# Kernel tuning notes

Measured on AMD Instinct MI355X. Metric: run time of the kernel, lower is better.

Reference implementation:

```python
import jax, jax.numpy as jnp
import numpy as np

N = 8192       # tokens = batch x seq
D = 2048       # d_model
H = 2048       # per-expert hidden size
E = 8          # num_experts
TOP_K = 2


def setup_inputs() -> dict:
    key = jax.random.key(0)
    ks = jax.random.split(key, 6)
    x = jax.random.normal(ks[0], (N, D), dtype=jnp.float32)
    expert_weights = jax.random.uniform(ks[1], (N, TOP_K), dtype=jnp.float32)
    expert_indices = jax.random.randint(ks[2], (N, TOP_K), 0, E, dtype=jnp.int32)
    batch_size_per_expert = jnp.bincount(expert_indices.reshape(-1), length=E).astype(jnp.int32)
    scale = 0.02
    w1 = jax.random.normal(ks[3], (E, D, H), dtype=jnp.float32) * scale
    w2 = jax.random.normal(ks[4], (E, H, D), dtype=jnp.float32) * scale
    w3 = jax.random.normal(ks[5], (E, D, H), dtype=jnp.float32) * scale
    return {"x": x, "expert_weights": expert_weights, "expert_indices": expert_indices,
            "batch_size_per_expert": batch_size_per_expert, "w1": w1, "w2": w2, "w3": w3}


def reference(x, expert_weights, expert_indices, batch_size_per_expert, w1, w2, w3):
    """Math-equivalent to ParallelMLP.forward_once (non-EP path):
    sort tokens by expert, run per-expert SwiGLU MLP, unpermute and combine
    with top-k routing weights. Output does not depend on the sort order,
    so we express it as: out[t] = sum_k w[t,k] * expert_{idx[t,k]}(x[t]).
    """
    n, d = x.shape
    e = w1.shape[0]
    # Dense combine weights (n, E): scatter top-k routing weights.
    cw = jnp.zeros((n, e), x.dtype).at[jnp.arange(n)[:, None], expert_indices].add(expert_weights)
    out = jnp.zeros_like(x)
    for i in range(e):  # small fixed expert count
        h = jax.nn.silu(x @ w1[i]) * (x @ w3[i])  # (n, H) SwiGLU
        out = out + cw[:, i:i + 1] * (h @ w2[i])
    return out
```

## Files before the change

kernel.cpp:

```cpp
#include <hip/hip_runtime.h>
#include <stdint.h>

typedef unsigned short u16;
typedef __attribute__((ext_vector_type(8))) short s16x8;
typedef __attribute__((ext_vector_type(8))) unsigned short u16x8;
typedef __attribute__((ext_vector_type(4))) float f32x4;

#define N_TOK 8192
#define DDIM 2048
#define HDIM 2048
#define NROWS 16384
#define PADROWS 16640
#define MAXTILES 72
#define KTILES 32

#define W1T_OFF    0ull
#define W3T_OFF    67108864ull
#define W2T_OFF    134217728ull
#define XBF_OFF    201326592ull
#define HS_OFF     234881024ull
#define ROWTOK_OFF 303038464ull
#define POS_OFF    303107072ull
#define META_OFF   303172608ull
#define RES_OFF    0ull
#define WS_NEED    303172736ull

__device__ __forceinline__ u16 f2bf(float f) {
  union { float f; unsigned u; } v; v.f = f;
  unsigned r = v.u + 0x7fffu + ((v.u >> 16) & 1u);
  return (u16)(r >> 16);
}
__device__ __forceinline__ float bf2f(u16 u) {
  union { unsigned u; float f; } v; v.u = ((unsigned)u) << 16; return v.f;
}
__device__ __forceinline__ void gload_lds16(const u16* g, u16* l) {
  __builtin_amdgcn_global_load_lds(
      (const __attribute__((address_space(1))) unsigned int*)g,
      (__attribute__((address_space(3))) unsigned int*)l, 16, 0, 0);
}

__global__ void r1_kernel(const int* __restrict__ bsz, int* __restrict__ meta,
                          int* __restrict__ rowtok) {
  if (threadIdx.x == 0) {
    int off = 0, tbv = 0;
    meta[8] = 0; meta[17] = 0;
    for (int e = 0; e < 8; ++e) {
      meta[e] = 0;
      int c = bsz[e];
      off += c;  meta[9 + e] = off;
      tbv += (c + 255) >> 8; meta[18 + e] = tbv;
    }
  }
  for (int p = NROWS + (int)threadIdx.x; p < PADROWS; p += 256) rowtok[p] = 0;
}

__global__ void r2_kernel(const int* __restrict__ eidx, int* __restrict__ meta,
                          int* __restrict__ rowtok, int* __restrict__ posOf) {
  int i = blockIdx.x * 256 + threadIdx.x;
  int e = eidx[i];
  int p = atomicAdd(&meta[e], 1);
  int row = meta[8 + e] + p;
  rowtok[row] = i >> 1;
  posOf[i] = row;
}

__global__ void convert_x_kernel(const float* __restrict__ x, u16* __restrict__ xbf) {
  long long c = blockIdx.x * 256 + threadIdx.x;
  const float4 v0 = *(const float4*)&x[c * 8];
  const float4 v1 = *(const float4*)&x[c * 8 + 4];
  u16x8 u;
  u[0] = f2bf(v0.x); u[1] = f2bf(v0.y); u[2] = f2bf(v0.z); u[3] = f2bf(v0.w);
  u[4] = f2bf(v1.x); u[5] = f2bf(v1.y); u[6] = f2bf(v1.z); u[7] = f2bf(v1.w);
  *(u16x8*)&xbf[c * 8] = u;
}

__global__ __launch_bounds__(256) void transpose_cvt_kernel(
    const float* __restrict__ w1, const float* __restrict__ w2, const float* __restrict__ w3,
    u16* __restrict__ w1T, u16* __restrict__ w2T, u16* __restrict__ w3T) {
  __shared__ float tile[64][65];
  int z = blockIdx.z;
  const float* src; u16* dst;
  if (z < 8)        { src = w1 + (size_t)z * 4194304;        dst = w1T + (size_t)z * 4194304; }
  else if (z < 16)  { src = w3 + (size_t)(z - 8) * 4194304;  dst = w3T + (size_t)(z - 8) * 4194304; }
  else              { src = w2 + (size_t)(z - 16) * 4194304; dst = w2T + (size_t)(z - 16) * 4194304; }
  int r0 = blockIdx.y * 64, c0 = blockIdx.x * 64;
  int tid = threadIdx.x;
  int lr = tid >> 4, lc4 = (tid & 15) * 4;
#pragma unroll
  for (int i = 0; i < 4; ++i) {
    const float4 v = *(const float4*)&src[(size_t)(r0 + lr + i * 16) * 2048 + c0 + lc4];
    tile[lr + i * 16][lc4 + 0] = v.x; tile[lr + i * 16][lc4 + 1] = v.y;
    tile[lr + i * 16][lc4 + 2] = v.z; tile[lr + i * 16][lc4 + 3] = v.w;
  }
  __syncthreads();
  int orb = tid >> 3, oc8 = (tid & 7) * 8;
#pragma unroll
  for (int i = 0; i < 2; ++i) {
    int orow = orb + i * 32;
    u16x8 u;
#pragma unroll
    for (int j = 0; j < 8; ++j) u[j] = f2bf(tile[oc8 + j][orow]);
    *(u16x8*)&dst[(size_t)(c0 + orow) * 2048 + r0 + oc8] = u;
  }
}

template<int EPI>
__global__ __launch_bounds__(512, 2) void gemm_moe_kernel(
    const u16* __restrict__ A, const u16* __restrict__ B1m, const u16* __restrict__ B3m,
    const int* __restrict__ gather, const int* __restrict__ meta, u16* __restrict__ out) {
  const int* offs = meta + 8;
  const int* tb = meta + 17;

  const int nwg = (int)(gridDim.x * gridDim.y);
  const int lin = (int)(blockIdx.y * gridDim.x + blockIdx.x);
  const int q8 = nwg >> 3, r8 = nwg & 7;
  const int xcd = lin & 7, idx = lin >> 3;
  const int nl = (xcd < r8 ? xcd * (q8 + 1) : r8 * (q8 + 1) + (xcd - r8) * q8) + idx;
  const int tileId = nl % MAXTILES;
  const int colb = nl / MAXTILES;

  if (tileId >= tb[8]) return;
  int e = 0;
#pragma unroll
  for (int qq = 1; qq < 8; ++qq) if (tileId >= tb[qq]) e = qq;
  const int row0 = offs[e] + (tileId - tb[e]) * 256;
  const int vr = offs[e + 1] - row0;

  const int bRowA = EPI ? colb * 128 : colb * 256;
  const int bRowB = EPI ? colb * 128 : colb * 256 + 128;

  __shared__ u16 lds[2][4][8192];

  const int tid = threadIdx.x;
  const int wid = tid >> 6, lane = tid & 63;
  const int lm = lane & 15, kg = lane >> 4;
  const int wr = wid >> 2, wc = wid & 3;

  const u16* pA0[2]; const u16* pA1[2]; const u16* pB1[2]; const u16* pB3[2];
#pragma unroll
  for (int l = 0; l < 2; ++l) {
    int S = (wid * 2 + l) * 64 + lane;
    int r = S >> 3;
    int c8 = ((S & 7) ^ (r & 7)) * 8;
    int ga0 = row0 + r, ga1 = row0 + 128 + r;
    int ta0 = gather ? gather[ga0] : ga0;
    int ta1 = gather ? gather[ga1] : ga1;
    pA0[l] = A + (size_t)ta0 * 2048 + c8;
    pA1[l] = A + (size_t)ta1 * 2048 + c8;
    pB1[l] = B1m + ((size_t)e * 2048 + bRowA + r) * 2048 + c8;
    pB3[l] = B3m + ((size_t)e * 2048 + bRowB + r) * 2048 + c8;
  }

  int fA[2];
  fA[0] = lm * 64 + ((kg) ^ (lm & 7)) * 8;
  fA[1] = lm * 64 + ((4 + kg) ^ (lm & 7)) * 8;

  f32x4 acc1[8][2], acc3[8][2];
  f32x4 z4 = {0.f, 0.f, 0.f, 0.f};
#pragma unroll
  for (int m = 0; m < 8; ++m)
#pragma unroll
    for (int n = 0; n < 2; ++n) { acc1[m][n] = z4; acc3[m][n] = z4; }

#define STG(b, u, P) do { \
    gload_lds16(P[0], &lds[b][u][(wid * 2 + 0) * 512]); \
    gload_lds16(P[1], &lds[b][u][(wid * 2 + 1) * 512]); } while (0)
#define ADV() do { pA0[0]+=64; pA0[1]+=64; pA1[0]+=64; pA1[1]+=64; \
    pB1[0]+=64; pB1[1]+=64; pB3[0]+=64; pB3[1]+=64; } while (0)

  STG(0, 0, pA0); STG(0, 1, pA1); STG(0, 2, pB1); STG(0, 3, pB3);
  ADV();
  asm volatile("s_waitcnt vmcnt(0)" ::: "memory");
  __builtin_amdgcn_s_barrier();

  s16x8 a[4][2], b[2][2];

  for (int t = 0; t < KTILES; ++t) {
    const int cur = t & 1;
    const bool more = (t + 1 < KTILES);

#pragma unroll
    for (int mi = 0; mi < 4; ++mi)
#pragma unroll
      for (int kk = 0; kk < 2; ++kk)
        a[mi][kk] = *(const s16x8*)&lds[cur][wr][mi * 1024 + fA[kk]];
#pragma unroll
    for (int n = 0; n < 2; ++n)
#pragma unroll
      for (int kk = 0; kk < 2; ++kk)
        b[n][kk] = *(const s16x8*)&lds[cur][2][wc * 2048 + n * 1024 + fA[kk]];
    if (more) { STG(cur ^ 1, 0, pA0); STG(cur ^ 1, 2, pB1); }
    __builtin_amdgcn_s_barrier();
    __builtin_amdgcn_s_setprio(1);
#pragma unroll
    for (int mi = 0; mi < 4; ++mi)
#pragma unroll
      for (int n = 0; n < 2; ++n) {
        acc1[mi][n] = __builtin_amdgcn_mfma_f32_16x16x32_bf16(a[mi][0], b[n][0], acc1[mi][n], 0, 0, 0);
        acc1[mi][n] = __builtin_amdgcn_mfma_f32_16x16x32_bf16(a[mi][1], b[n][1], acc1[mi][n], 0, 0, 0);
      }
    __builtin_amdgcn_s_setprio(0);
    __builtin_amdgcn_s_barrier();

#pragma unroll
    for (int n = 0; n < 2; ++n)
#pragma unroll
      for (int kk = 0; kk < 2; ++kk)
        b[n][kk] = *(const s16x8*)&lds[cur][3][wc * 2048 + n * 1024 + fA[kk]];
    if (more) { STG(cur ^ 1, 1, pA1); STG(cur ^ 1, 3, pB3); }
    __builtin_amdgcn_s_barrier();
    __builtin_amdgcn_s_setprio(1);
#pragma unroll
    for (int mi = 0; mi < 4; ++mi)
#pragma unroll
      for (int n = 0; n < 2; ++n) {
        acc3[mi][n] = __builtin_amdgcn_mfma_f32_16x16x32_bf16(a[mi][0], b[n][0], acc3[mi][n], 0, 0, 0);
        acc3[mi][n] = __builtin_amdgcn_mfma_f32_16x16x32_bf16(a[mi][1], b[n][1], acc3[mi][n], 0, 0, 0);
      }
    __builtin_amdgcn_s_setprio(0);
    __builtin_amdgcn_s_barrier();

#pragma unroll
    for (int mi = 0; mi < 4; ++mi)
#pragma unroll
      for (int kk = 0; kk < 2; ++kk)
        a[mi][kk] = *(const s16x8*)&lds[cur][wr][(4 + mi) * 1024 + fA[kk]];
#pragma unroll
    for (int n = 0; n < 2; ++n)
#pragma unroll
      for (int kk = 0; kk < 2; ++kk)
        b[n][kk] = *(const s16x8*)&lds[cur][2][wc * 2048 + n * 1024 + fA[kk]];
    __builtin_amdgcn_s_barrier();
    __builtin_amdgcn_s_setprio(1);
#pragma unroll
    for (int mi = 0; mi < 4; ++mi)
#pragma unroll
      for (int n = 0; n < 2; ++n) {
        acc1[4 + mi][n] = __builtin_amdgcn_mfma_f32_16x16x32_bf16(a[mi][0], b[n][0], acc1[4 + mi][n], 0, 0, 0);
        acc1[4 + mi][n] = __builtin_amdgcn_mfma_f32_16x16x32_bf16(a[mi][1], b[n][1], acc1[4 + mi][n], 0, 0, 0);
      }
    __builtin_amdgcn_s_setprio(0);
    __builtin_amdgcn_s_barrier();

#pragma unroll
    for (int n = 0; n < 2; ++n)
#pragma unroll
      for (int kk = 0; kk < 2; ++kk)
        b[n][kk] = *(const s16x8*)&lds[cur][3][wc * 2048 + n * 1024 + fA[kk]];
    asm volatile("s_waitcnt vmcnt(0)" ::: "memory");
    __builtin_amdgcn_s_barrier();
    __builtin_amdgcn_s_setprio(1);
#pragma unroll
    for (int mi = 0; mi < 4; ++mi)
#pragma unroll
      for (int n = 0; n < 2; ++n) {
        acc3[4 + mi][n] = __builtin_amdgcn_mfma_f32_16x16x32_bf16(a[mi][0], b[n][0], acc3[4 + mi][n], 0, 0, 0);
        acc3[4 + mi][n] = __builtin_amdgcn_mfma_f32_16x16x32_bf16(a[mi][1], b[n][1], acc3[4 + mi][n], 0, 0, 0);
      }
    __builtin_amdgcn_s_setprio(0);
    __builtin_amdgcn_s_barrier();

    if (more) ADV();
  }

#pragma unroll
  for (int m = 0; m < 8; ++m)
#pragma unroll
    for (int n = 0; n < 2; ++n) {
      const int rloc = wr * 128 + m * 16 + kg * 4;
      if (EPI == 1) {
        const int col = colb * 128 + wc * 32 + n * 16 + lm;
#pragma unroll
        for (int rr = 0; rr < 4; ++rr) {
          int rowl = rloc + rr;
          if (rowl < vr) {
            float z = acc1[m][n][rr];
            float h = z / (1.f + __expf(-z)) * acc3[m][n][rr];
            out[(size_t)(row0 + rowl) * 2048 + col] = f2bf(h);
          }
        }
      } else {
        const int col = colb * 256 + wc * 32 + n * 16 + lm;
#pragma unroll
        for (int rr = 0; rr < 4; ++rr) {
          int rowl = rloc + rr;
          if (rowl < vr) {
            out[(size_t)(row0 + rowl) * 2048 + col] = f2bf(acc1[m][n][rr]);
            out[(size_t)(row0 + rowl) * 2048 + col + 128] = f2bf(acc3[m][n][rr]);
          }
        }
      }
    }
#undef STG
#undef ADV
}

__global__ void combine_kernel(const u16* __restrict__ res, const int* __restrict__ posOf,
                               const float* __restrict__ ew, float* __restrict__ out) {
  int c = blockIdx.x * 256 + threadIdx.x;
  int t = c >> 8, dc = (c & 255) * 8;
  int p0 = posOf[2 * t], p1 = posOf[2 * t + 1];
  float wa = ew[2 * t], wb = ew[2 * t + 1];
  u16x8 u0 = *(const u16x8*)&res[(size_t)p0 * 2048 + dc];
  u16x8 u1 = *(const u16x8*)&res[(size_t)p1 * 2048 + dc];
  float4 o0, o1;
  o0.x = wa * bf2f(u0[0]) + wb * bf2f(u1[0]);
  o0.y = wa * bf2f(u0[1]) + wb * bf2f(u1[1]);
  o0.z = wa * bf2f(u0[2]) + wb * bf2f(u1[2]);
  o0.w = wa * bf2f(u0[3]) + wb * bf2f(u1[3]);
  o1.x = wa * bf2f(u0[4]) + wb * bf2f(u1[4]);
  o1.y = wa * bf2f(u0[5]) + wb * bf2f(u1[5]);
  o1.z = wa * bf2f(u0[6]) + wb * bf2f(u1[6]);
  o1.w = wa * bf2f(u0[7]) + wb * bf2f(u1[7]);
  *(float4*)&out[(size_t)t * 2048 + dc] = o0;
  *(float4*)&out[(size_t)t * 2048 + dc + 4] = o1;
}

extern "C" void kernel_launch(void* const* d_in, const int* in_sizes, int n_in,
                              void* d_out, int out_size, void* d_ws, size_t ws_size,
                              hipStream_t stream) {
  const float* x  = (const float*)d_in[0];
  const float* ew = (const float*)d_in[1];
  const int* eidx = (const int*)d_in[2];
  const int* bsz  = (const int*)d_in[3];
  const float* w1 = (const float*)d_in[4];
  const float* w2 = (const float*)d_in[5];
  const float* w3 = (const float*)d_in[6];
  float* out = (float*)d_out;
  char* ws = (char*)d_ws;

  if (ws_size < WS_NEED) {
    hipMemsetAsync(d_out, 0, (size_t)out_size * 4, stream);
    return;
  }

  u16* w1T = (u16*)(ws + W1T_OFF);
  u16* w3T = (u16*)(ws + W3T_OFF);
  u16* w2T = (u16*)(ws + W2T_OFF);
  u16* xbf = (u16*)(ws + XBF_OFF);
  u16* hs  = (u16*)(ws + HS_OFF);
  u16* res = (u16*)(ws + RES_OFF);
  int* rowtok = (int*)(ws + ROWTOK_OFF);
  int* posOf  = (int*)(ws + POS_OFF);
  int* meta   = (int*)(ws + META_OFF);

  r1_kernel<<<1, 256, 0, stream>>>(bsz, meta, rowtok);
  r2_kernel<<<64, 256, 0, stream>>>(eidx, meta, rowtok, posOf);
  convert_x_kernel<<<8192, 256, 0, stream>>>(x, xbf);
  transpose_cvt_kernel<<<dim3(32, 32, 24), 256, 0, stream>>>(w1, w2, w3, w1T, w2T, w3T);
  gemm_moe_kernel<1><<<dim3(MAXTILES, 16), 512, 0, stream>>>(xbf, w1T, w3T, rowtok, meta, hs);
  gemm_moe_kernel<0><<<dim3(MAXTILES, 8), 512, 0, stream>>>(hs, w2T, w2T, nullptr, meta, res);
  combine_kernel<<<8192, 256, 0, stream>>>(res, posOf, ew, out);
}
```

Baseline: 762.9 us.

## Prefetch full next K-tile up front and cut barriers in MoE GEMM loop

The GEMM main loop is restructured so all eight global-to-LDS loads for the next K-tile are issued at the start of each iteration. A partial `s_waitcnt vmcnt(8)` then waits only for the current tile, and the loop body drops from eight barriers to three. B1 and B3 fragments are read from LDS together so each A fragment feeds both accumulators in one MFMA burst, and the last iteration is peeled off. This aims to reduce barrier stalls and give loads more time to overlap compute. The cost is extra live B registers under the 512x2 launch bound, which could cause spills or lower occupancy.

```diff
diff --git a/kernel.cpp b/kernel.cpp
--- a/kernel.cpp
+++ b/kernel.cpp
@@ -105,7 +105,7 @@
 }
 
 template<int EPI>
-__global__ __launch_bounds__(512, 2) void gemm_moe_kernel(
+__device__ __forceinline__ void gemm_body(
     const u16* __restrict__ A, const u16* __restrict__ B1m, const u16* __restrict__ B3m,
     const int* __restrict__ gather, const int* __restrict__ meta, u16* __restrict__ out) {
   const int* offs = meta + 8;
@@ -165,102 +165,68 @@
 #define STG(b, u, P) do { \
     gload_lds16(P[0], &lds[b][u][(wid * 2 + 0) * 512]); \
     gload_lds16(P[1], &lds[b][u][(wid * 2 + 1) * 512]); } while (0)
+#define STG_ALL(b) do { STG(b, 0, pA0); STG(b, 1, pA1); \
+    STG(b, 2, pB1); STG(b, 3, pB3); } while (0)
 #define ADV() do { pA0[0]+=64; pA0[1]+=64; pA1[0]+=64; pA1[1]+=64; \
     pB1[0]+=64; pB1[1]+=64; pB3[0]+=64; pB3[1]+=64; } while (0)
 
-  STG(0, 0, pA0); STG(0, 1, pA1); STG(0, 2, pB1); STG(0, 3, pB3);
+  STG_ALL(0);
   ADV();
-  asm volatile("s_waitcnt vmcnt(0)" ::: "memory");
-  __builtin_amdgcn_s_barrier();
-
-  s16x8 a[4][2], b[2][2];
-
-  for (int t = 0; t < KTILES; ++t) {
+
+  s16x8 a[4][2], b1r[2][2], b3r[2][2];
+
+#define READ_B() do { \
+_Pragma("unroll") \
+    for (int n = 0; n < 2; ++n) \
+_Pragma("unroll") \
+      for (int kk = 0; kk < 2; ++kk) { \
+        b1r[n][kk] = *(const s16x8*)&lds[cur][2][wc * 2048 + n * 1024 + fA[kk]]; \
+        b3r[n][kk] = *(const s16x8*)&lds[cur][3][wc * 2048 + n * 1024 + fA[kk]]; \
+      } } while (0)
+#define READ_A(half) do { \
+_Pragma("unroll") \
+    for (int mi = 0; mi < 4; ++mi) \
+_Pragma("unroll") \
+      for (int kk = 0; kk < 2; ++kk) \
+        a[mi][kk] = *(const s16x8*)&lds[cur][wr][((half) * 4 + mi) * 1024 + fA[kk]]; \
+    } while (0)
+#define MFMA32(half) do { \
+    __builtin_amdgcn_s_setprio(1); \
+_Pragma("unroll") \
+    for (int mi = 0; mi < 4; ++mi) \
+_Pragma("unroll") \
+      for (int n = 0; n < 2; ++n) { \
+        acc1[(half)*4+mi][n] = __builtin_amdgcn_mfma_f32_16x16x32_bf16(a[mi][0], b1r[n][0], acc1[(half)*4+mi][n], 0, 0, 0); \
+        acc1[(half)*4+mi][n] = __builtin_amdgcn_mfma_f32_16x16x32_bf16(a[mi][1], b1r[n][1], acc1[(half)*4+mi][n], 0, 0, 0); \
+        acc3[(half)*4+mi][n] = __builtin_amdgcn_mfma_f32_16x16x32_bf16(a[mi][0], b3r[n][0], acc3[(half)*4+mi][n], 0, 0, 0); \
+        acc3[(half)*4+mi][n] = __builtin_amdgcn_mfma_f32_16x16x32_bf16(a[mi][1], b3r[n][1], acc3[(half)*4+mi][n], 0, 0, 0); \
+      } \
+    __builtin_amdgcn_s_setprio(0); } while (0)
+
+  for (int t = 0; t < KTILES - 1; ++t) {
     const int cur = t & 1;
-    const bool more = (t + 1 < KTILES);
-
-#pragma unroll
-    for (int mi = 0; mi < 4; ++mi)
-#pragma unroll
-      for (int kk = 0; kk < 2; ++kk)
-        a[mi][kk] = *(const s16x8*)&lds[cur][wr][mi * 1024 + fA[kk]];
-#pragma unroll
-    for (int n = 0; n < 2; ++n)
-#pragma unroll
-      for (int kk = 0; kk < 2; ++kk)
-        b[n][kk] = *(const s16x8*)&lds[cur][2][wc * 2048 + n * 1024 + fA[kk]];
-    if (more) { STG(cur ^ 1, 0, pA0); STG(cur ^ 1, 2, pB1); }
-    __builtin_amdgcn_s_barrier();
-    __builtin_amdgcn_s_setprio(1);
-#pragma unroll
-    for (int mi = 0; mi < 4; ++mi)
-#pragma unroll
-      for (int n = 0; n < 2; ++n) {
-        acc1[mi][n] = __builtin_amdgcn_mfma_f32_16x16x32_bf16(a[mi][0], b[n][0], acc1[mi][n], 0, 0, 0);
-        acc1[mi][n] = __builtin_amdgcn_mfma_f32_16x16x32_bf16(a[mi][1], b[n][1], acc1[mi][n], 0, 0, 0);
-      }
-    __builtin_amdgcn_s_setprio(0);
-    __builtin_amdgcn_s_barrier();
-
-#pragma unroll
-    for (int n = 0; n < 2; ++n)
-#pragma unroll
-      for (int kk = 0; kk < 2; ++kk)
-        b[n][kk] = *(const s16x8*)&lds[cur][3][wc * 2048 + n * 1024 + fA[kk]];
-    if (more) { STG(cur ^ 1, 1, pA1); STG(cur ^ 1, 3, pB3); }
-    __builtin_amdgcn_s_barrier();
-    __builtin_amdgcn_s_setprio(1);
-#pragma unroll
-    for (int mi = 0; mi < 4; ++mi)
-#pragma unroll
-      for (int n = 0; n < 2; ++n) {
-        acc3[mi][n] = __builtin_amdgcn_mfma_f32_16x16x32_bf16(a[mi][0], b[n][0], acc3[mi][n], 0, 0, 0);
-        acc3[mi][n] = __builtin_amdgcn_mfma_f32_16x16x32_bf16(a[mi][1], b[n][1], acc3[mi][n], 0, 0, 0);
-      }
-    __builtin_amdgcn_s_setprio(0);
-    __builtin_amdgcn_s_barrier();
-
-#pragma unroll
-    for (int mi = 0; mi < 4; ++mi)
-#pragma unroll
-      for (int kk = 0; kk < 2; ++kk)
-        a[mi][kk] = *(const s16x8*)&lds[cur][wr][(4 + mi) * 1024 + fA[kk]];
-#pragma unroll
-    for (int n = 0; n < 2; ++n)
-#pragma unroll
-      for (int kk = 0; kk < 2; ++kk)
-        b[n][kk] = *(const s16x8*)&lds[cur][2][wc * 2048 + n * 1024 + fA[kk]];
-    __builtin_amdgcn_s_barrier();
-    __builtin_amdgcn_s_setprio(1);
-#pragma unroll
-    for (int mi = 0; mi < 4; ++mi)
-#pragma unroll
-      for (int n = 0; n < 2; ++n) {
-        acc1[4 + mi][n] = __builtin_amdgcn_mfma_f32_16x16x32_bf16(a[mi][0], b[n][0], acc1[4 + mi][n], 0, 0, 0);
-        acc1[4 + mi][n] = __builtin_amdgcn_mfma_f32_16x16x32_bf16(a[mi][1], b[n][1], acc1[4 + mi][n], 0, 0, 0);
-      }
-    __builtin_amdgcn_s_setprio(0);
-    __builtin_amdgcn_s_barrier();
-
-#pragma unroll
-    for (int n = 0; n < 2; ++n)
-#pragma unroll
-      for (int kk = 0; kk < 2; ++kk)
-        b[n][kk] = *(const s16x8*)&lds[cur][3][wc * 2048 + n * 1024 + fA[kk]];
+    STG_ALL(cur ^ 1);
+    ADV();
+    asm volatile("s_waitcnt vmcnt(8)" ::: "memory");
+    __builtin_amdgcn_s_barrier();
+    READ_A(0);
+    READ_B();
+    MFMA32(0);
+    __builtin_amdgcn_s_barrier();
+    READ_A(1);
+    MFMA32(1);
+    __builtin_amdgcn_s_barrier();
+  }
+  {
+    const int cur = (KTILES - 1) & 1;
     asm volatile("s_waitcnt vmcnt(0)" ::: "memory");
     __builtin_amdgcn_s_barrier();
-    __builtin_amdgcn_s_setprio(1);
-#pragma unroll
-    for (int mi = 0; mi < 4; ++mi)
-#pragma unroll
-      for (int n = 0; n < 2; ++n) {
-        acc3[4 + mi][n] = __builtin_amdgcn_mfma_f32_16x16x32_bf16(a[mi][0], b[n][0], acc3[4 + mi][n], 0, 0, 0);
-        acc3[4 + mi][n] = __builtin_amdgcn_mfma_f32_16x16x32_bf16(a[mi][1], b[n][1], acc3[4 + mi][n], 0, 0, 0);
-      }
-    __builtin_amdgcn_s_setprio(0);
-    __builtin_amdgcn_s_barrier();
-
-    if (more) ADV();
+    READ_A(0);
+    READ_B();
+    MFMA32(0);
+    __builtin_amdgcn_s_barrier();
+    READ_A(1);
+    MFMA32(1);
   }
 
 #pragma unroll
@@ -292,7 +258,22 @@
       }
     }
 #undef STG
+#undef STG_ALL
 #undef ADV
+#undef READ_B
+#undef READ_A
+#undef MFMA32
+}
+
+__global__ __launch_bounds__(512, 2) void gemm1_kernel(
+    const u16* __restrict__ A, const u16* __restrict__ B1m, const u16* __restrict__ B3m,
+    const int* __restrict__ gather, const int* __restrict__ meta, u16* __restrict__ out) {
+  gemm_body<1>(A, B1m, B3m, gather, meta, out);
+}
+__global__ __launch_bounds__(512, 2) void gemm2_kernel(
+    const u16* __restrict__ A, const u16* __restrict__ B1m, const u16* __restrict__ B3m,
+    const int* __restrict__ gather, const int* __restrict__ meta, u16* __restrict__ out) {
+  gemm_body<0>(A, B1m, B3m, gather, meta, out);
 }
 
 __global__ void combine_kernel(const u16* __restrict__ res, const int* __restrict__ posOf,
@@ -348,7 +329,7 @@
   r2_kernel<<<64, 256, 0, stream>>>(eidx, meta, rowtok, posOf);
   convert_x_kernel<<<8192, 256, 0, stream>>>(x, xbf);
   transpose_cvt_kernel<<<dim3(32, 32, 24), 256, 0, stream>>>(w1, w2, w3, w1T, w2T, w3T);
-  gemm_moe_kernel<1><<<dim3(MAXTILES, 16), 512, 0, stream>>>(xbf, w1T, w3T, rowtok, meta, hs);
-  gemm_moe_kernel<0><<<dim3(MAXTILES, 8), 512, 0, stream>>>(hs, w2T, w2T, nullptr, meta, res);
+  gemm1_kernel<<<dim3(MAXTILES, 16), 512, 0, stream>>>(xbf, w1T, w3T, rowtok, meta, hs);
+  gemm2_kernel<<<dim3(MAXTILES, 8), 512, 0, stream>>>(hs, w2T, w2T, nullptr, meta, res);
   combine_kernel<<<8192, 256, 0, stream>>>(res, posOf, ew, out);
 }
```

Result: faster. 730.4 us (-4.3%).
